# Performance work log

Hardware: AMD Instinct MI355X
Metric: run time of the kernel (lower is better)

Reference implementation:

```python
import math
import jax, jax.numpy as jnp
import numpy as np

B, T, C, H = 2, 2048, 1024, 16
HD = C // H  # head dim = 64
EPS_LN = 1e-5
EPS_ENT = 1e-8


def layer_norm(x, w, b):
    mu = jnp.mean(x, axis=-1, keepdims=True)
    var = jnp.var(x, axis=-1, keepdims=True)
    return (x - mu) * jax.lax.rsqrt(var + EPS_LN) * w + b


def new_gelu(x):
    c = math.sqrt(2.0 / math.pi)
    return 0.5 * x * (1.0 + jnp.tanh(c * (x + 0.044715 * x * x * x)))


def setup_inputs() -> dict:
    key = jax.random.key(0)
    ks = jax.random.split(key, 8)
    s = 0.02
    return {
        "x": jax.random.normal(ks[0], (B, T, C), dtype=jnp.float32),
        "ln1_w": jnp.ones((C,), jnp.float32),
        "ln1_b": jnp.zeros((C,), jnp.float32),
        "w_attn": jax.random.normal(ks[1], (3 * C, C), jnp.float32) * s,
        "b_attn": jnp.zeros((3 * C,), jnp.float32),
        "w_proj": jax.random.normal(ks[2], (C, C), jnp.float32) * s,
        "b_proj": jnp.zeros((C,), jnp.float32),
        "ln2_w": jnp.ones((C,), jnp.float32),
        "ln2_b": jnp.zeros((C,), jnp.float32),
        "w_fc": jax.random.normal(ks[3], (4 * C, C), jnp.float32) * s,
        "b_fc": jnp.zeros((4 * C,), jnp.float32),
        "w_mlp": jax.random.normal(ks[4], (C, 4 * C), jnp.float32) * s,
        "b_mlp": jnp.zeros((C,), jnp.float32),
    }


def reference(x, ln1_w, ln1_b, w_attn, b_attn, w_proj, b_proj,
              ln2_w, ln2_b, w_fc, b_fc, w_mlp, b_mlp):
    # --- attention branch (pre-LN) ---
    h = layer_norm(x, ln1_w, ln1_b)
    qkv = h @ w_attn.T + b_attn                      # (B,T,3C)
    q, k, v = jnp.split(qkv, 3, axis=-1)
    # (B,T,C) -> (B,H,T,HD)
    q = q.reshape(B, T, H, HD).transpose(0, 2, 1, 3)
    k = k.reshape(B, T, H, HD).transpose(0, 2, 1, 3)
    v = v.reshape(B, T, H, HD).transpose(0, 2, 1, 3)

    att = jnp.einsum('bhqd,bhkd->bhqk', q, k) * (1.0 / math.sqrt(HD))
    causal = jnp.tril(jnp.ones((T, T), dtype=bool))
    att = jnp.where(causal, att, -jnp.inf)
    att = jax.nn.softmax(att, axis=-1)               # (B,H,T,T)
    # entropy per query, averaged over batch/heads/positions -> scalar
    att_entropy = jnp.mean(jnp.sum(-att * jnp.log(att + EPS_ENT), axis=-1))

    y = jnp.einsum('bhqk,bhkd->bhqd', att, v)        # (B,H,T,HD)
    y = y.transpose(0, 2, 1, 3).reshape(B, T, C)
    y = y @ w_proj.T + b_proj
    x = x + y

    # --- MLP branch ---
    h2 = layer_norm(x, ln2_w, ln2_b)
    m = new_gelu(h2 @ w_fc.T + b_fc) @ w_mlp.T + b_mlp
    x = x + m

    present = jnp.stack([k, v])                      # (2,B,H,T,HD)
    return (x, att_entropy, present)
```

## Files before the change

### kernel.cpp

```cpp
#include <hip/hip_runtime.h>
#include <hip/hip_bf16.h>
#include <stdint.h>


typedef __bf16 bf16x8 __attribute__((ext_vector_type(8)));
typedef __bf16 bf16x4 __attribute__((ext_vector_type(4)));
typedef float  f32x4  __attribute__((ext_vector_type(4)));

#define GLDS16(g, l)                                                          \
  __builtin_amdgcn_global_load_lds(                                           \
      (__attribute__((address_space(1))) void*)(g),                           \
      (__attribute__((address_space(3))) void*)(l), 16, 0, 0)

__device__ __forceinline__ float gelu_f(float x) {
  float u2 = 1.5957691216057308f * (x + 0.044715f * x * x * x);
  return x * __builtin_amdgcn_rcpf(1.0f + __expf(-u2));
}

__global__ __launch_bounds__(256) void cast_w(
    const float* s0, const float* s1, const float* s2, const float* s3,
    __bf16* d0, __bf16* d1, __bf16* d2, __bf16* d3,
    int n0, int n1, int n2, int n3) {
  int a = blockIdx.y;
  const float* s = (a == 0) ? s0 : (a == 1) ? s1 : (a == 2) ? s2 : s3;
  __bf16* d      = (a == 0) ? d0 : (a == 1) ? d1 : (a == 2) ? d2 : d3;
  int n          = (a == 0) ? n0 : (a == 1) ? n1 : (a == 2) ? n2 : n3;
  int i = (blockIdx.x * 256 + threadIdx.x) * 4;
  if (i < n) {
    float4 v = *(const float4*)(s + i);
    bf16x4 o = {(__bf16)v.x, (__bf16)v.y, (__bf16)v.z, (__bf16)v.w};
    *(bf16x4*)(d + i) = o;
  }
}

__global__ __launch_bounds__(256) void ln_kernel(
    const float* __restrict__ x, const float* __restrict__ gw,
    const float* __restrict__ gb, __bf16* __restrict__ out) {
  const int row = blockIdx.x, tid = threadIdx.x;
  const float4 v = ((const float4*)(x + (size_t)row * 1024))[tid];
  float s = v.x + v.y + v.z + v.w;
  float sq = v.x * v.x + v.y * v.y + v.z * v.z + v.w * v.w;
#pragma unroll
  for (int m = 1; m < 64; m <<= 1) {
    s += __shfl_xor(s, m, 64);
    sq += __shfl_xor(sq, m, 64);
  }
  __shared__ float red[8];
  if ((tid & 63) == 0) { red[tid >> 6] = s; red[4 + (tid >> 6)] = sq; }
  __syncthreads();
  s = red[0] + red[1] + red[2] + red[3];
  sq = red[4] + red[5] + red[6] + red[7];
  const float mu = s * (1.0f / 1024.0f);
  const float var = sq * (1.0f / 1024.0f) - mu * mu;
  const float rs = rsqrtf(var + 1e-5f);
  const float4 wv = ((const float4*)gw)[tid];
  const float4 bv = ((const float4*)gb)[tid];
  bf16x4 o;
  o[0] = (__bf16)((v.x - mu) * rs * wv.x + bv.x);
  o[1] = (__bf16)((v.y - mu) * rs * wv.y + bv.y);
  o[2] = (__bf16)((v.z - mu) * rs * wv.z + bv.z);
  o[3] = (__bf16)((v.w - mu) * rs * wv.w + bv.w);
  *(bf16x4*)(out + (size_t)row * 1024 + tid * 4) = o;
}

template <int EPI, int BN>
__global__ __launch_bounds__(256) void gemm_bt(
    const __bf16* __restrict__ A, const __bf16* __restrict__ Bw,
    const float* __restrict__ bias, const float* __restrict__ resid,
    float* __restrict__ outF, __bf16* __restrict__ outH, int M, int N, int K) {
  __shared__ __bf16 As[128 * 32];
  __shared__ __bf16 Bs[BN * 32];
  constexpr int JN = BN / 32;
  const int tid = threadIdx.x;
  const int w = tid >> 6, lane = tid & 63, l15 = lane & 15, quad = lane >> 4;
  const int wm = (w >> 1) * 64, wn = (w & 1) * (BN / 2);
  const int m0 = blockIdx.y * 128, n0 = blockIdx.x * BN;
  const int arow = tid >> 2, acol = (tid & 3) * 8;

  f32x4 acc[4][JN] = {};

  const __bf16* ga = A + (size_t)(m0 + arow) * K + acol;
  const __bf16* gb = Bw + (size_t)(n0 + arow) * K + acol;
  for (int k0 = 0; k0 < K; k0 += 32) {
    __syncthreads();
    GLDS16(ga + k0, (char*)As + tid * 16);
    GLDS16(ga + k0 + (size_t)64 * K, (char*)As + 4096 + tid * 16);
    GLDS16(gb + k0, (char*)Bs + tid * 16);
    if (BN == 128)
      GLDS16(gb + k0 + (size_t)64 * K, (char*)Bs + 4096 + tid * 16);
    __syncthreads();
    bf16x8 af[4], bfr[JN];
#pragma unroll
    for (int i = 0; i < 4; ++i)
      af[i] = *(const bf16x8*)(As + (wm + i * 16 + l15) * 32 + quad * 8);
#pragma unroll
    for (int j = 0; j < JN; ++j)
      bfr[j] = *(const bf16x8*)(Bs + (wn + j * 16 + l15) * 32 + quad * 8);
#pragma unroll
    for (int i = 0; i < 4; ++i)
#pragma unroll
      for (int j = 0; j < JN; ++j)
        acc[i][j] = __builtin_amdgcn_mfma_f32_16x16x32_bf16(bfr[j], af[i],
                                                            acc[i][j], 0, 0, 0);
  }
#pragma unroll
  for (int j = 0; j < JN; ++j) {
    const int nb = n0 + wn + j * 16 + quad * 4;
    const float4 bv = *(const float4*)(bias + nb);
#pragma unroll
    for (int i = 0; i < 4; ++i) {
      const int m = m0 + wm + i * 16 + l15;
      const size_t idx = (size_t)m * N + nb;
      const float v0 = acc[i][j][0] + bv.x;
      const float v1 = acc[i][j][1] + bv.y;
      const float v2 = acc[i][j][2] + bv.z;
      const float v3 = acc[i][j][3] + bv.w;
      if (EPI == 0) {
        bf16x4 o = {(__bf16)v0, (__bf16)v1, (__bf16)v2, (__bf16)v3};
        *(bf16x4*)(outH + idx) = o;
      } else if (EPI == 1) {
        const float4 rv = *(const float4*)(resid + idx);
        float4 o = {v0 + rv.x, v1 + rv.y, v2 + rv.z, v3 + rv.w};
        *(float4*)(outF + idx) = o;
      } else {
        bf16x4 o = {(__bf16)gelu_f(v0), (__bf16)gelu_f(v1), (__bf16)gelu_f(v2),
                    (__bf16)gelu_f(v3)};
        *(bf16x4*)(outH + idx) = o;
      }
    }
  }
}

__global__ __launch_bounds__(256) void prep_kernel(
    const __bf16* __restrict__ qkv, __bf16* __restrict__ Qb,
    __bf16* __restrict__ Kb, __bf16* __restrict__ Vtb,
    float* __restrict__ pres) {
  const int tt = blockIdx.x, bh = blockIdx.y;
  const int b = bh >> 4, h = bh & 15;
  const int t0 = tt * 64, tid = threadIdx.x;
  const int r = tid >> 2, c = (tid & 3) * 16;
  __shared__ __bf16 Vs[64 * 72];

  const __bf16* base = qkv + (size_t)(b * 2048 + t0 + r) * 3072 + h * 64 + c;
  bf16x8 q0 = *(const bf16x8*)(base);
  bf16x8 q1 = *(const bf16x8*)(base + 8);
  bf16x8 k0 = *(const bf16x8*)(base + 1024);
  bf16x8 k1 = *(const bf16x8*)(base + 1032);
  bf16x8 v0 = *(const bf16x8*)(base + 2048);
  bf16x8 v1 = *(const bf16x8*)(base + 2056);

  const size_t orow = ((size_t)bh * 2048 + t0 + r) * 64 + c;
  *(bf16x8*)(Qb + orow) = q0;
  *(bf16x8*)(Qb + orow + 8) = q1;
  *(bf16x8*)(Kb + orow) = k0;
  *(bf16x8*)(Kb + orow + 8) = k1;

  float* pk = pres + (((size_t)(b * 16 + h)) * 2048 + t0 + r) * 64 + c;
  float* pv = pk + (size_t)2 * 16 * 2048 * 64;
#pragma unroll
  for (int i = 0; i < 4; ++i) {
    float4 fk = {(float)k0[i * 4 + 0], (float)k0[i * 4 + 1],
                 (float)k0[i * 4 + 2], (float)k0[i * 4 + 3]};
    float4 fv = {(float)v0[i * 4 + 0], (float)v0[i * 4 + 1],
                 (float)v0[i * 4 + 2], (float)v0[i * 4 + 3]};
    if (i >= 2) {
      fk = {(float)k1[i * 4 - 8], (float)k1[i * 4 - 7], (float)k1[i * 4 - 6],
            (float)k1[i * 4 - 5]};
      fv = {(float)v1[i * 4 - 8], (float)v1[i * 4 - 7], (float)v1[i * 4 - 6],
            (float)v1[i * 4 - 5]};
    }
    ((float4*)pk)[i] = fk;
    ((float4*)pv)[i] = fv;
  }

  *(bf16x8*)(Vs + r * 72 + c) = v0;
  *(bf16x8*)(Vs + r * 72 + c + 8) = v1;
  __syncthreads();
  const int d = tid >> 2, tc = (tid & 3) * 16;
  bf16x8 o0, o1;
#pragma unroll
  for (int i = 0; i < 8; ++i) {
    o0[i] = Vs[(tc + i) * 72 + d];
    o1[i] = Vs[(tc + 8 + i) * 72 + d];
  }
  __bf16* vo = Vtb + ((size_t)bh * 64 + d) * 2048 + t0 + tc;
  *(bf16x8*)(vo) = o0;
  *(bf16x8*)(vo + 8) = o1;
}

__global__ __launch_bounds__(256) void attn_kernel(
    const __bf16* __restrict__ Qb, const __bf16* __restrict__ Kb,
    const __bf16* __restrict__ Vtb, __bf16* __restrict__ attn_out,
    float* __restrict__ ent_acc) {
  const int qp = blockIdx.x;
  const int bh = blockIdx.y;
  const int b = bh >> 4, h = bh & 15;
  const int tid = threadIdx.x, w = tid >> 6, lane = tid & 63;
  const int l15 = lane & 15, quad = lane >> 4;

  __shared__ __bf16 Ks[64 * 72];
  __shared__ __bf16 Vt[64 * 72];
  __shared__ __bf16 Ps[64 * 72];
  __shared__ float entred[4];

  const __bf16* qbase = Qb + (size_t)bh * 2048 * 64;
  const __bf16* kbase = Kb + (size_t)bh * 2048 * 64;
  const __bf16* vbase = Vtb + (size_t)bh * 64 * 2048;

  const int sr = tid >> 2, sc = (tid & 3) * 16;

  float hacc = 0.f;

#pragma unroll 1
  for (int ph = 0; ph < 2; ++ph) {
    const int qt = ph ? (31 - qp) : qp;
    const int q0 = qt * 64;
    const int qrow = q0 + w * 16 + l15;
    bf16x8 qf[2];
#pragma unroll
    for (int s = 0; s < 2; ++s)
      qf[s] = *(const bf16x8*)(qbase + (size_t)qrow * 64 + s * 32 + quad * 8);

    f32x4 O[4] = {};
    float m_s = -1e30f, l_s = 0.f, r_s = 0.f;

    for (int kt = 0; kt <= qt; ++kt) {
      const int kk0 = kt * 64;
      __syncthreads();
      {
        bf16x8 k0 = *(const bf16x8*)(kbase + (size_t)(kk0 + sr) * 64 + sc);
        bf16x8 k1 = *(const bf16x8*)(kbase + (size_t)(kk0 + sr) * 64 + sc + 8);
        bf16x8 v0 = *(const bf16x8*)(vbase + (size_t)sr * 2048 + kk0 + sc);
        bf16x8 v1 = *(const bf16x8*)(vbase + (size_t)sr * 2048 + kk0 + sc + 8);
        *(bf16x8*)(Ks + sr * 72 + sc) = k0;
        *(bf16x8*)(Ks + sr * 72 + sc + 8) = k1;
        *(bf16x8*)(Vt + sr * 72 + sc) = v0;
        *(bf16x8*)(Vt + sr * 72 + sc + 8) = v1;
      }
      __syncthreads();

      f32x4 sacc[4] = {};
#pragma unroll
      for (int s = 0; s < 2; ++s)
#pragma unroll
        for (int jt = 0; jt < 4; ++jt) {
          bf16x8 kf =
              *(const bf16x8*)(Ks + (jt * 16 + l15) * 72 + s * 32 + quad * 8);
          sacc[jt] =
              __builtin_amdgcn_mfma_f32_16x16x32_bf16(kf, qf[s], sacc[jt], 0, 0, 0);
        }

      float sv[4][4], ev[4][4];
#pragma unroll
      for (int jt = 0; jt < 4; ++jt)
#pragma unroll
        for (int r = 0; r < 4; ++r) {
          float xv = sacc[jt][r] * 0.125f;
          if (kk0 + jt * 16 + quad * 4 + r > qrow) xv = -1e30f;
          sv[jt][r] = xv;
        }
      float mx = sv[0][0];
#pragma unroll
      for (int jt = 0; jt < 4; ++jt)
#pragma unroll
        for (int r = 0; r < 4; ++r) mx = fmaxf(mx, sv[jt][r]);
      mx = fmaxf(mx, __shfl_xor(mx, 16, 64));
      mx = fmaxf(mx, __shfl_xor(mx, 32, 64));
      const float mn = fmaxf(m_s, mx);
      const float al = __expf(m_s - mn);
      m_s = mn;
      float ls = 0.f, rs2 = 0.f;
#pragma unroll
      for (int jt = 0; jt < 4; ++jt)
#pragma unroll
        for (int r = 0; r < 4; ++r) {
          const float e = __expf(sv[jt][r] - mn);
          ev[jt][r] = e;
          ls += e;
          rs2 = fmaf(e, sv[jt][r], rs2);
        }
      ls += __shfl_xor(ls, 16, 64);
      rs2 += __shfl_xor(rs2, 16, 64);
      ls += __shfl_xor(ls, 32, 64);
      rs2 += __shfl_xor(rs2, 32, 64);
      l_s = l_s * al + ls;
      r_s = r_s * al + rs2;
#pragma unroll
      for (int jt = 0; jt < 4; ++jt)
#pragma unroll
        for (int r = 0; r < 4; ++r) O[jt][r] *= al;

      __bf16* prow = Ps + (w * 16 + l15) * 72;
#pragma unroll
      for (int jt = 0; jt < 4; ++jt) {
        bf16x4 pk = {(__bf16)ev[jt][0], (__bf16)ev[jt][1], (__bf16)ev[jt][2],
                     (__bf16)ev[jt][3]};
        *(bf16x4*)(prow + jt * 16 + quad * 4) = pk;
      }
      asm volatile("s_waitcnt lgkmcnt(0)" ::: "memory");
#pragma unroll
      for (int s = 0; s < 2; ++s) {
        bf16x8 pf = *(const bf16x8*)(prow + s * 32 + quad * 8);
#pragma unroll
        for (int jt = 0; jt < 4; ++jt) {
          bf16x8 vf =
              *(const bf16x8*)(Vt + (jt * 16 + l15) * 72 + s * 32 + quad * 8);
          O[jt] = __builtin_amdgcn_mfma_f32_16x16x32_bf16(vf, pf, O[jt], 0, 0, 0);
        }
      }
    }

    const float inv = 1.0f / l_s;
    __bf16* obase = attn_out + (size_t)(b * 2048 + qrow) * 1024 + h * 64;
#pragma unroll
    for (int jt = 0; jt < 4; ++jt) {
      bf16x4 ov = {(__bf16)(O[jt][0] * inv), (__bf16)(O[jt][1] * inv),
                   (__bf16)(O[jt][2] * inv), (__bf16)(O[jt][3] * inv)};
      *(bf16x4*)(obase + jt * 16 + quad * 4) = ov;
    }
    hacc += m_s + __logf(l_s) - r_s * inv;
  }

#pragma unroll
  for (int m = 1; m < 64; m <<= 1) hacc += __shfl_xor(hacc, m, 64);
  if (lane == 0) entred[w] = hacc;
  __syncthreads();
  if (tid == 0)
    atomicAdd(ent_acc, (entred[0] + entred[1] + entred[2] + entred[3]) *
                           (1.0f / (4.0f * 65536.0f)));
}

__global__ void ent_final(const float* __restrict__ e, float* __restrict__ o) {
  if (threadIdx.x == 0) o[0] = e[0];
}

extern "C" void kernel_launch(void* const* d_in, const int* in_sizes, int n_in,
                              void* d_out, int out_size, void* d_ws,
                              size_t ws_size, hipStream_t stream) {
  const float* x      = (const float*)d_in[0];
  const float* ln1_w  = (const float*)d_in[1];
  const float* ln1_b  = (const float*)d_in[2];
  const float* w_attn = (const float*)d_in[3];
  const float* b_attn = (const float*)d_in[4];
  const float* w_proj = (const float*)d_in[5];
  const float* b_proj = (const float*)d_in[6];
  const float* ln2_w  = (const float*)d_in[7];
  const float* ln2_b  = (const float*)d_in[8];
  const float* w_fc   = (const float*)d_in[9];
  const float* b_fc   = (const float*)d_in[10];
  const float* w_mlp  = (const float*)d_in[11];
  const float* b_mlp  = (const float*)d_in[12];

  char* ws = (char*)d_ws;
  constexpr size_t MB = 1024ull * 1024ull;
  __bf16* qkv    = (__bf16*)(ws + 0);
  __bf16* act    = (__bf16*)(ws + 0);
  __bf16* wbattn = (__bf16*)(ws + 24 * MB);
  __bf16* wbproj = (__bf16*)(ws + 30 * MB);
  __bf16* attnb  = (__bf16*)(ws + 32 * MB);
  __bf16* hb     = (__bf16*)(ws + 40 * MB);
  __bf16* Vtb    = (__bf16*)(ws + 40 * MB);
  __bf16* Qb     = (__bf16*)(ws + 48 * MB);
  __bf16* Kb     = (__bf16*)(ws + 56 * MB);
  float*  x2     = (float*)(ws + 48 * MB);
  __bf16* wbfc   = (__bf16*)(ws + 64 * MB);
  __bf16* wbmlp  = (__bf16*)(ws + 72 * MB);
  float*  entw   = (float*)(ws + 80 * MB);

  float* xout   = (float*)d_out;
  float* entout = xout + 4194304;
  float* pres   = xout + 4194305;

  hipMemsetAsync(entw, 0, sizeof(float), stream);
  cast_w<<<dim3(4096, 4), 256, 0, stream>>>(
      w_attn, w_proj, w_fc, w_mlp, wbattn, wbproj, wbfc, wbmlp,
      3 * 1024 * 1024, 1024 * 1024, 4 * 1024 * 1024, 4 * 1024 * 1024);
  ln_kernel<<<4096, 256, 0, stream>>>(x, ln1_w, ln1_b, hb);
  gemm_bt<0, 128><<<dim3(24, 32), 256, 0, stream>>>(
      hb, wbattn, b_attn, nullptr, nullptr, qkv, 4096, 3072, 1024);
  prep_kernel<<<dim3(32, 32), 256, 0, stream>>>(qkv, Qb, Kb, Vtb, pres);
  attn_kernel<<<dim3(16, 32), 256, 0, stream>>>(Qb, Kb, Vtb, attnb, entw);
  gemm_bt<1, 64><<<dim3(16, 32), 256, 0, stream>>>(
      attnb, wbproj, b_proj, x, x2, nullptr, 4096, 1024, 1024);
  ln_kernel<<<4096, 256, 0, stream>>>(x2, ln2_w, ln2_b, hb);
  gemm_bt<2, 128><<<dim3(32, 32), 256, 0, stream>>>(
      hb, wbfc, b_fc, nullptr, nullptr, act, 4096, 4096, 1024);
  gemm_bt<1, 64><<<dim3(16, 32), 256, 0, stream>>>(
      act, wbmlp, b_mlp, x2, xout, nullptr, 4096, 1024, 4096);
  ent_final<<<1, 64, 0, stream>>>(entw, entout);
}
```

Baseline: 427.4 us.

## Double GEMM K-step per barrier, add XCD-aware block remap and occupancy hints

The GEMM kernel now loads two 32-wide K slices per iteration into separate LDS buffers, which halves the number of barrier pairs and issues more loads per sync. GEMM and attention blocks are remapped so that consecutive block IDs, which are spread round-robin across XCDs, share row tiles or heads on the same XCD for better L2 reuse. Launch bounds now carry a min-waves hint per instantiation. The cost is twice the LDS per block, and the occupancy hint may push the compiler toward register limits or spills.

```diff
diff --git a/kernel.cpp b/kernel.cpp
--- a/kernel.cpp
+++ b/kernel.cpp
@@ -63,58 +63,70 @@
   *(bf16x4*)(out + (size_t)row * 1024 + tid * 4) = o;
 }
 
-template <int EPI, int BN>
-__global__ __launch_bounds__(256) void gemm_bt(
+template <int EPI, int BN, int MINW>
+__global__ __launch_bounds__(256, MINW) void gemm_bt(
     const __bf16* __restrict__ A, const __bf16* __restrict__ Bw,
     const float* __restrict__ bias, const float* __restrict__ resid,
     float* __restrict__ outF, __bf16* __restrict__ outH, int M, int N, int K) {
-  __shared__ __bf16 As[128 * 32];
-  __shared__ __bf16 Bs[BN * 32];
+  __shared__ __bf16 As[2][128 * 32];
+  __shared__ __bf16 Bs[2][BN * 32];
   constexpr int JN = BN / 32;
   const int tid = threadIdx.x;
   const int w = tid >> 6, lane = tid & 63, l15 = lane & 15, quad = lane >> 4;
   const int wm = (w >> 1) * 64, wn = (w & 1) * (BN / 2);
-  const int m0 = blockIdx.y * 128, n0 = blockIdx.x * BN;
+  const int nx = gridDim.x;
+  const int j = blockIdx.y * nx + blockIdx.x;
+  const int xcd = j & 7, u = j >> 3;
+  const int yl = u / nx, xx = u - yl * nx;
+  const int yy = xcd * (gridDim.y >> 3) + yl;
+  const int m0 = yy * 128, n0 = xx * BN;
   const int arow = tid >> 2, acol = (tid & 3) * 8;
 
   f32x4 acc[4][JN] = {};
 
   const __bf16* ga = A + (size_t)(m0 + arow) * K + acol;
   const __bf16* gb = Bw + (size_t)(n0 + arow) * K + acol;
-  for (int k0 = 0; k0 < K; k0 += 32) {
+  for (int k0 = 0; k0 < K; k0 += 64) {
     __syncthreads();
-    GLDS16(ga + k0, (char*)As + tid * 16);
-    GLDS16(ga + k0 + (size_t)64 * K, (char*)As + 4096 + tid * 16);
-    GLDS16(gb + k0, (char*)Bs + tid * 16);
-    if (BN == 128)
-      GLDS16(gb + k0 + (size_t)64 * K, (char*)Bs + 4096 + tid * 16);
+#pragma unroll
+    for (int h = 0; h < 2; ++h) {
+      GLDS16(ga + k0 + h * 32, (char*)As[h] + tid * 16);
+      GLDS16(ga + k0 + h * 32 + (size_t)64 * K, (char*)As[h] + 4096 + tid * 16);
+      GLDS16(gb + k0 + h * 32, (char*)Bs[h] + tid * 16);
+      if (BN == 128)
+        GLDS16(gb + k0 + h * 32 + (size_t)64 * K,
+               (char*)Bs[h] + 4096 + tid * 16);
+    }
     __syncthreads();
-    bf16x8 af[4], bfr[JN];
-#pragma unroll
-    for (int i = 0; i < 4; ++i)
-      af[i] = *(const bf16x8*)(As + (wm + i * 16 + l15) * 32 + quad * 8);
-#pragma unroll
-    for (int j = 0; j < JN; ++j)
-      bfr[j] = *(const bf16x8*)(Bs + (wn + j * 16 + l15) * 32 + quad * 8);
-#pragma unroll
-    for (int i = 0; i < 4; ++i)
-#pragma unroll
-      for (int j = 0; j < JN; ++j)
-        acc[i][j] = __builtin_amdgcn_mfma_f32_16x16x32_bf16(bfr[j], af[i],
-                                                            acc[i][j], 0, 0, 0);
-  }
-#pragma unroll
-  for (int j = 0; j < JN; ++j) {
-    const int nb = n0 + wn + j * 16 + quad * 4;
+#pragma unroll
+    for (int h = 0; h < 2; ++h) {
+      bf16x8 af[4], bfr[JN];
+#pragma unroll
+      for (int i = 0; i < 4; ++i)
+        af[i] = *(const bf16x8*)(As[h] + (wm + i * 16 + l15) * 32 + quad * 8);
+#pragma unroll
+      for (int j2 = 0; j2 < JN; ++j2)
+        bfr[j2] = *(const bf16x8*)(Bs[h] + (wn + j2 * 16 + l15) * 32 + quad * 8);
+#pragma unroll
+      for (int i = 0; i < 4; ++i)
+#pragma unroll
+        for (int j2 = 0; j2 < JN; ++j2)
+          acc[i][j2] = __builtin_amdgcn_mfma_f32_16x16x32_bf16(
+              bfr[j2], af[i], acc[i][j2], 0, 0, 0);
+    }
+  }
+#pragma unroll
+  for (int j2 = 0; j2 < JN; ++j2) {
+    const int nb = n0 + wn + j2 * 16 + quad * 4;
     const float4 bv = *(const float4*)(bias + nb);
 #pragma unroll
     for (int i = 0; i < 4; ++i) {
       const int m = m0 + wm + i * 16 + l15;
       const size_t idx = (size_t)m * N + nb;
-      const float v0 = acc[i][j][0] + bv.x;
-      const float v1 = acc[i][j][1] + bv.y;
-      const float v2 = acc[i][j][2] + bv.z;
-      const float v3 = acc[i][j][3] + bv.w;
+      const float v0 = acc[i][j2][0] + bv.x;
+      const float v1 = acc[i][j2][1] + bv.y;
+      const float v2 = acc[i][j2][2] + bv.z;
+      const float v3 = acc[i][j2][3] + bv.w;
       if (EPI == 0) {
         bf16x4 o = {(__bf16)v0, (__bf16)v1, (__bf16)v2, (__bf16)v3};
         *(bf16x4*)(outH + idx) = o;
@@ -192,8 +204,10 @@
     const __bf16* __restrict__ Qb, const __bf16* __restrict__ Kb,
     const __bf16* __restrict__ Vtb, __bf16* __restrict__ attn_out,
     float* __restrict__ ent_acc) {
-  const int qp = blockIdx.x;
-  const int bh = blockIdx.y;
+  const int jlin = blockIdx.y * 16 + blockIdx.x;
+  const int xcd = jlin & 7, u = jlin >> 3;
+  const int qp = u & 15;
+  const int bh = xcd * 4 + (u >> 4);
   const int b = bh >> 4, h = bh & 15;
   const int tid = threadIdx.x, w = tid >> 6, lane = tid & 63;
   const int l15 = lane & 15, quad = lane >> 4;
@@ -376,16 +390,16 @@
       w_attn, w_proj, w_fc, w_mlp, wbattn, wbproj, wbfc, wbmlp,
       3 * 1024 * 1024, 1024 * 1024, 4 * 1024 * 1024, 4 * 1024 * 1024);
   ln_kernel<<<4096, 256, 0, stream>>>(x, ln1_w, ln1_b, hb);
-  gemm_bt<0, 128><<<dim3(24, 32), 256, 0, stream>>>(
+  gemm_bt<0, 128, 4><<<dim3(24, 32), 256, 0, stream>>>(
       hb, wbattn, b_attn, nullptr, nullptr, qkv, 4096, 3072, 1024);
   prep_kernel<<<dim3(32, 32), 256, 0, stream>>>(qkv, Qb, Kb, Vtb, pres);
   attn_kernel<<<dim3(16, 32), 256, 0, stream>>>(Qb, Kb, Vtb, attnb, entw);
-  gemm_bt<1, 64><<<dim3(16, 32), 256, 0, stream>>>(
+  gemm_bt<1, 64, 2><<<dim3(16, 32), 256, 0, stream>>>(
       attnb, wbproj, b_proj, x, x2, nullptr, 4096, 1024, 1024);
   ln_kernel<<<4096, 256, 0, stream>>>(x2, ln2_w, ln2_b, hb);
-  gemm_bt<2, 128><<<dim3(32, 32), 256, 0, stream>>>(
+  gemm_bt<2, 128, 4><<<dim3(32, 32), 256, 0, stream>>>(
       hb, wbfc, b_fc, nullptr, nullptr, act, 4096, 4096, 1024);
-  gemm_bt<1, 64><<<dim3(16, 32), 256, 0, stream>>>(
+  gemm_bt<1, 64, 2><<<dim3(16, 32), 256, 0, stream>>>(
       act, wbmlp, b_mlp, x2, xout, nullptr, 4096, 1024, 4096);
   ent_final<<<1, 64, 0, stream>>>(entw, entout);
 }
```

Result: faster. 383.2 us (-10.3%).
